# Optimization experiments

Hardware: AMD Instinct MI355X
Metric: run time of the kernel (lower is better)

Reference implementation:

```python
import jax, jax.numpy as jnp
import numpy as np

N = 50000      # nodes
E = 800000     # edges (avg degree 16)
IN = 128       # in_dim = num_heads * out_dim
H = 8          # num_heads
D = 16         # out_dim per head
R = 9          # num_rels = num_bases


def setup_inputs() -> dict:
    key = jax.random.key(0)
    ks = jax.random.split(key, 13)
    sw = 1.0 / np.sqrt(IN)
    sc = 1.0 / np.sqrt(R)
    return {
        "h": jax.random.normal(ks[0], (N, IN), jnp.float32),
        "Qw": jax.random.normal(ks[1], (R, IN, IN), jnp.float32) * sw,
        "Qc": jax.random.normal(ks[2], (R, R), jnp.float32) * sc,
        "Qb": jax.random.normal(ks[3], (IN,), jnp.float32) * 0.02,
        "Kw": jax.random.normal(ks[4], (R, IN, IN), jnp.float32) * sw,
        "Kc": jax.random.normal(ks[5], (R, R), jnp.float32) * sc,
        "Kb": jax.random.normal(ks[6], (IN,), jnp.float32) * 0.02,
        "Vw": jax.random.normal(ks[7], (R, IN, IN), jnp.float32) * sw,
        "Vc": jax.random.normal(ks[8], (R, R), jnp.float32) * sc,
        "Vb": jax.random.normal(ks[9], (IN,), jnp.float32) * 0.02,
        "src": jax.random.randint(ks[10], (E,), 0, N, jnp.int32),
        "dst": jax.random.randint(ks[11], (E,), 0, N, jnp.int32),
        "etype": jax.random.randint(ks[12], (E,), 0, R, jnp.int32),
    }


def _rel_graph_conv(x, w_basis, comb, bias, src, dst, etype):
    # basis decomposition: W_r = sum_b comb[r,b] * basis[b]  -> [R, IN, IN]
    W = jnp.einsum("rb,bio->rio", comb, w_basis)
    # project node features under every relation once: [R, N, IN]
    xW = jnp.einsum("ni,rio->rno", x, W)
    # per-edge message m_e = W_{etype_e} x_{src_e}
    msg = xW[etype, src]                                   # [E, IN]
    agg = jax.ops.segment_sum(msg, dst, num_segments=N)    # sum over incoming edges
    return jax.nn.relu(agg + bias)                         # dropout = eval mode (identity)


def reference(h, Qw, Qc, Qb, Kw, Kc, Kb, Vw, Vc, Vb, src, dst, etype):
    Q = _rel_graph_conv(h, Qw, Qc, Qb, src, dst, etype).reshape(N, H, D)
    K = _rel_graph_conv(h, Kw, Kc, Kb, src, dst, etype).reshape(N, H, D)
    V = _rel_graph_conv(h, Vw, Vc, Vb, src, dst, etype).reshape(N, H, D)
    # edge attention score: (K_src . Q_dst) per head, scaled + clamped exp
    score = jnp.sum(K[src] * Q[dst], axis=-1, keepdims=True) / np.sqrt(D)  # [E, H, 1]
    score = jnp.exp(jnp.clip(score, -10.0, 10.0))
    # weighted-V aggregation and normalizer via segment sums over dst
    wV = jax.ops.segment_sum(V[src] * score, dst, num_segments=N)  # [N, H, D]
    z = jax.ops.segment_sum(score, dst, num_segments=N)            # [N, H, 1]
    return wV / (z + 1e-6)
```

## Files before the change

### kernel.cpp

```cpp
#include <hip/hip_runtime.h>

#define NN 50000
#define NE 800000
#define IND 128
#define NH 8
#define DH 16
#define NR 9
#define KTOT 1152
#define NOUT 384
#define OB_N 24
#define NBLK 196

typedef __attribute__((ext_vector_type(8))) short bf16x8;
typedef __attribute__((ext_vector_type(4))) float f32x4;

__device__ __forceinline__ ushort f2bf(float x) {
  unsigned u = __float_as_uint(x);
  u += 0x7FFF + ((u >> 16) & 1);
  return (ushort)(u >> 16);
}
__device__ __forceinline__ float bf2f(ushort h) {
  return __uint_as_float(((unsigned)h) << 16);
}

__global__ __launch_bounds__(256) void make_w(const float* __restrict__ Qw, const float* __restrict__ Qc,
                                              const float* __restrict__ Kw, const float* __restrict__ Kc,
                                              const float* __restrict__ Vw, const float* __restrict__ Vc,
                                              ushort* __restrict__ Wh, ushort* __restrict__ Wl) {
  int t = blockIdx.x * 256 + threadIdx.x;
  int k = t / NOUT;
  int og = t % NOUT;
  int r = k >> 7, i = k & 127;
  int m = og >> 7, oc = og & 127;
  const float* basis = m == 0 ? Qw : m == 1 ? Kw : Vw;
  const float* comb  = m == 0 ? Qc : m == 1 ? Kc : Vc;
  float w = 0.f;
#pragma unroll
  for (int b = 0; b < NR; ++b)
    w += comb[r * NR + b] * basis[(long)b * IND * IND + i * IND + oc];
  ushort hi = f2bf(w);
  ushort lo = f2bf(w - bf2f(hi));
  long idx = ((long)(k >> 5) * OB_N + (og >> 4)) * 512
           + (((k >> 3) & 3) * 16 + (og & 15)) * 8 + (k & 7);
  Wh[idx] = hi;
  Wl[idx] = lo;
}

__global__ __launch_bounds__(256) void hist_dst(const int* __restrict__ dst,
                                                int* __restrict__ deg) {
  int e = blockIdx.x * 256 + threadIdx.x;
  if (e < NE) atomicAdd(&deg[dst[e]], 1);
}

__global__ __launch_bounds__(256) void scan_p1(const int* __restrict__ deg,
                                               int* __restrict__ bsum) {
  __shared__ int sb[256];
  int t = threadIdx.x;
  int idx = blockIdx.x * 256 + t;
  int v = (idx < NN) ? deg[idx] : 0;
  sb[t] = v;
  __syncthreads();
  for (int off = 128; off > 0; off >>= 1) {
    if (t < off) sb[t] += sb[t + off];
    __syncthreads();
  }
  if (t == 0) bsum[blockIdx.x] = sb[0];
}

__global__ __launch_bounds__(256) void scan_p2(const int* __restrict__ bsum,
                                               int* __restrict__ boff,
                                               int* __restrict__ rowptr) {
  __shared__ int sb[256];
  int t = threadIdx.x;
  int v = (t < NBLK) ? bsum[t] : 0;
  sb[t] = v;
  __syncthreads();
  for (int off = 1; off < 256; off <<= 1) {
    int add = (t >= off) ? sb[t - off] : 0;
    __syncthreads();
    sb[t] += add;
    __syncthreads();
  }
  if (t < NBLK) boff[t] = sb[t] - v;
  if (t == 0) rowptr[NN] = NE;
}

__global__ __launch_bounds__(256) void scan_p3(const int* __restrict__ deg,
                                               const int* __restrict__ boff,
                                               int* __restrict__ rowptr,
                                               int* __restrict__ cursor) {
  __shared__ int sb[256];
  int t = threadIdx.x;
  int idx = blockIdx.x * 256 + t;
  int v = (idx < NN) ? deg[idx] : 0;
  sb[t] = v;
  __syncthreads();
  for (int off = 1; off < 256; off <<= 1) {
    int add = (t >= off) ? sb[t - off] : 0;
    __syncthreads();
    sb[t] += add;
    __syncthreads();
  }
  if (idx < NN) {
    int excl = sb[t] - v + boff[blockIdx.x];
    rowptr[idx] = excl;
    cursor[idx] = excl;
  }
}

__global__ __launch_bounds__(256) void bucket_edges(const int* __restrict__ src,
                                                    const int* __restrict__ dst,
                                                    const int* __restrict__ et,
                                                    int* __restrict__ cursor,
                                                    int* __restrict__ epk) {
  int e = blockIdx.x * 256 + threadIdx.x;
  if (e >= NE) return;
  int d = dst[e];
  int pos = atomicAdd(&cursor[d], 1);
  epk[pos] = src[e] | (et[e] << 20);
}

__global__ __launch_bounds__(256) void conv_agg(const float* __restrict__ x,
                                                const int* __restrict__ rowptr,
                                                const int* __restrict__ epk,
                                                ushort* __restrict__ Ah,
                                                ushort* __restrict__ Al,
                                                int rlo, int rhi) {
  int wid = (blockIdx.x * 256 + threadIdx.x) >> 6;
  int lane = threadIdx.x & 63;
  if (wid >= NN) return;
  float ax[NR], ay[NR];
#pragma unroll
  for (int rr = 0; rr < NR; ++rr) { ax[rr] = 0.f; ay[rr] = 0.f; }
  int r0 = rowptr[wid], r1 = rowptr[wid + 1];
  for (int base = r0; base < r1; base += 64) {
    int pe = (base + lane < r1) ? epk[base + lane] : 0;
    int cnt = min(64, r1 - base);
    for (int j = 0; j < cnt; ++j) {
      int p = __shfl(pe, j);
      int s = p & 0xFFFFF;
      int r = p >> 20;
      float2 xv = *(const float2*)(x + (long)s * IND + lane * 2);
#pragma unroll
      for (int rr = 0; rr < NR; ++rr)
        if (r == rr) { ax[rr] += xv.x; ay[rr] += xv.y; }
    }
  }
#pragma unroll
  for (int rr = 0; rr < NR; ++rr)
    if (rr >= rlo && rr < rhi) {
      ushort h0 = f2bf(ax[rr]);
      ushort l0 = f2bf(ax[rr] - bf2f(h0));
      ushort h1 = f2bf(ay[rr]);
      ushort l1 = f2bf(ay[rr] - bf2f(h1));
      long o = ((long)(rr - rlo) * NN + wid) * IND + lane * 2;
      *(unsigned*)(Ah + o) = (unsigned)h0 | ((unsigned)h1 << 16);
      *(unsigned*)(Al + o) = (unsigned)l0 | ((unsigned)l1 << 16);
    }
}

__global__ __launch_bounds__(512) void gemm_mfma(const ushort* __restrict__ Ah,
                                                 const ushort* __restrict__ Al,
                                                 const ushort* __restrict__ Wh,
                                                 const ushort* __restrict__ Wl,
                                                 const float* __restrict__ Qb,
                                                 const float* __restrict__ Kb,
                                                 const float* __restrict__ Vb,
                                                 float* __restrict__ F,
                                                 int nrel, int rlo, int first, int last) {
  const int tid = threadIdx.x;
  const int lane = tid & 63;
  const int wid = tid >> 6;
  const int wr = wid >> 2;
  const int wc = wid & 3;
  const int n0 = blockIdx.x * 64 + wr * 32;
  const int l15 = lane & 15;
  const int kg = lane >> 4;

  const int rowA = min(n0 + l15, NN - 1);
  const int rowB = min(n0 + 16 + l15, NN - 1);

  f32x4 acc[2][6];
#pragma unroll
  for (int mi = 0; mi < 2; ++mi)
#pragma unroll
    for (int ni = 0; ni < 6; ++ni) acc[mi][ni] = (f32x4){0.f, 0.f, 0.f, 0.f};

  for (int c = 0; c < nrel; ++c) {
    const long aoff0 = ((long)c * NN + rowA) * IND + kg * 8;
    const long aoff1 = ((long)c * NN + rowB) * IND + kg * 8;
    const int kbg0 = (rlo + c) * 4;
#pragma unroll
    for (int kbl = 0; kbl < 4; ++kbl) {
      bf16x8 ah0 = *(const bf16x8*)(Ah + aoff0 + kbl * 32);
      bf16x8 ah1 = *(const bf16x8*)(Ah + aoff1 + kbl * 32);
      bf16x8 al0 = *(const bf16x8*)(Al + aoff0 + kbl * 32);
      bf16x8 al1 = *(const bf16x8*)(Al + aoff1 + kbl * 32);
#pragma unroll
      for (int ni = 0; ni < 6; ++ni) {
        const long boff = ((long)((kbg0 + kbl) * OB_N + wc * 6 + ni) * 64 + lane) * 8;
        bf16x8 bh = *(const bf16x8*)(Wh + boff);
        bf16x8 bl = *(const bf16x8*)(Wl + boff);
        acc[0][ni] = __builtin_amdgcn_mfma_f32_16x16x32_bf16(ah0, bl, acc[0][ni], 0, 0, 0);
        acc[0][ni] = __builtin_amdgcn_mfma_f32_16x16x32_bf16(al0, bh, acc[0][ni], 0, 0, 0);
        acc[0][ni] = __builtin_amdgcn_mfma_f32_16x16x32_bf16(ah0, bh, acc[0][ni], 0, 0, 0);
        acc[1][ni] = __builtin_amdgcn_mfma_f32_16x16x32_bf16(ah1, bl, acc[1][ni], 0, 0, 0);
        acc[1][ni] = __builtin_amdgcn_mfma_f32_16x16x32_bf16(al1, bh, acc[1][ni], 0, 0, 0);
        acc[1][ni] = __builtin_amdgcn_mfma_f32_16x16x32_bf16(ah1, bh, acc[1][ni], 0, 0, 0);
      }
    }
  }

#pragma unroll
  for (int mi = 0; mi < 2; ++mi) {
#pragma unroll
    for (int ni = 0; ni < 6; ++ni) {
      int og = wc * 96 + ni * 16 + l15;
      int m = og >> 7, oc = og & 127;
      float b = (m == 0 ? Qb : m == 1 ? Kb : Vb)[oc];
      float* Fm = F + (long)m * NN * IND;
#pragma unroll
      for (int reg = 0; reg < 4; ++reg) {
        int n = n0 + mi * 16 + kg * 4 + reg;
        if (n < NN) {
          long fo = (long)n * IND + oc;
          float v = acc[mi][ni][reg];
          if (!first) v += Fm[fo];
          if (last) { v += b; v = v > 0.f ? v : 0.f; }
          Fm[fo] = v;
        }
      }
    }
  }
}

__global__ __launch_bounds__(256) void node_attn(const float* __restrict__ Q,
                                                 const float* __restrict__ K,
                                                 const float* __restrict__ V,
                                                 const int* __restrict__ rowptr,
                                                 const int* __restrict__ epk,
                                                 float* __restrict__ out) {
  int wid = (blockIdx.x * 256 + threadIdx.x) >> 6;
  int lane = threadIdx.x & 63;
  if (wid >= NN) return;
  float2 q = *(const float2*)(Q + (long)wid * IND + lane * 2);
  float accx = 0.f, accy = 0.f, zacc = 0.f;
  int r0 = rowptr[wid], r1 = rowptr[wid + 1];
  for (int base = r0; base < r1; base += 64) {
    int pe = (base + lane < r1) ? epk[base + lane] : 0;
    int cnt = min(64, r1 - base);
    for (int j = 0; j < cnt; ++j) {
      int s = __shfl(pe, j) & 0xFFFFF;
      float2 k = *(const float2*)(K + (long)s * IND + lane * 2);
      float2 v = *(const float2*)(V + (long)s * IND + lane * 2);
      float p = q.x * k.x + q.y * k.y;
      p += __shfl_xor(p, 1);
      p += __shfl_xor(p, 2);
      p += __shfl_xor(p, 4);
      float score = __expf(fminf(fmaxf(p * 0.25f, -10.f), 10.f));
      accx += score * v.x;
      accy += score * v.y;
      zacc += score;
    }
  }
  float inv = 1.f / (zacc + 1e-6f);
  *(float2*)(out + (long)wid * IND + lane * 2) = make_float2(accx * inv, accy * inv);
}

extern "C" void kernel_launch(void* const* d_in, const int* in_sizes, int n_in,
                              void* d_out, int out_size, void* d_ws, size_t ws_size,
                              hipStream_t stream) {
  const float* h  = (const float*)d_in[0];
  const float* Qw = (const float*)d_in[1];
  const float* Qc = (const float*)d_in[2];
  const float* Qb = (const float*)d_in[3];
  const float* Kw = (const float*)d_in[4];
  const float* Kc = (const float*)d_in[5];
  const float* Kb = (const float*)d_in[6];
  const float* Vw = (const float*)d_in[7];
  const float* Vc = (const float*)d_in[8];
  const float* Vb = (const float*)d_in[9];
  const int* src = (const int*)d_in[10];
  const int* dst = (const int*)d_in[11];
  const int* et  = (const int*)d_in[12];
  float* out = (float*)d_out;

  char* p = (char*)d_ws;
  ushort* Wh = (ushort*)p;  p += (long)KTOT * NOUT * 2;
  ushort* Wl = (ushort*)p;  p += (long)KTOT * NOUT * 2;
  float* F   = (float*)p;   p += 3L * NN * IND * 4;
  int* deg    = (int*)p;
  int* rowptr = deg + NN;
  int* cursor = rowptr + NN + 1;
  int* bsum   = cursor + NN;
  int* boff   = bsum + NBLK;
  int* epk    = boff + NBLK;
  long intbytes = (((long)(3 * NN + 1 + 2 * NBLK + NE)) * 4 + 15) & ~15L;
  p += intbytes;
  ushort* Ah = (ushort*)p;
  long fixed = (long)(p - (char*)d_ws);
  long per_rel = 2L * NN * IND * 2;
  int C = (int)(((long)ws_size - fixed) / per_rel);
  if (C > NR) C = NR;
  if (C < 1) C = 1;
  ushort* Al = Ah + (long)C * NN * IND;

  hipMemsetAsync(deg, 0, (size_t)NN * 4, stream);

  make_w<<<(KTOT * NOUT) / 256, 256, 0, stream>>>(Qw, Qc, Kw, Kc, Vw, Vc, Wh, Wl);

  const int eb = (NE + 255) / 256;
  hist_dst<<<eb, 256, 0, stream>>>(dst, deg);
  scan_p1<<<NBLK, 256, 0, stream>>>(deg, bsum);
  scan_p2<<<1, 256, 0, stream>>>(bsum, boff, rowptr);
  scan_p3<<<NBLK, 256, 0, stream>>>(deg, boff, rowptr, cursor);
  bucket_edges<<<eb, 256, 0, stream>>>(src, dst, et, cursor, epk);

  const int nwb = (NN * 64 + 255) / 256;
  const int gb  = (NN + 63) / 64;

  int first = 1;
  for (int rlo = 0; rlo < NR; rlo += C) {
    int rhi = rlo + C;
    if (rhi > NR) rhi = NR;
    conv_agg<<<nwb, 256, 0, stream>>>(h, rowptr, epk, Ah, Al, rlo, rhi);
    gemm_mfma<<<gb, 512, 0, stream>>>(Ah, Al, Wh, Wl, Qb, Kb, Vb, F,
                                      rhi - rlo, rlo, first, (rhi == NR) ? 1 : 0);
    first = 0;
  }

  node_attn<<<nwb, 256, 0, stream>>>(F, F + (long)NN * IND, F + 2L * NN * IND,
                                     rowptr, epk, out);
}
```

Before: 915.3 us.

## Double the GEMM row tile and software-pipeline A/W register loads

The MFMA GEMM now covers 128 rows per block (64 per wave row) instead of 64, so each weight fragment loaded is reused across four row tiles rather than two. The K loop is flattened into steps and double-buffered in registers, with the next A and W fragments loaded while the current MFMAs run, to hide global-load latency. In exchange, register pressure rises considerably (96 accumulator floats plus fragment buffers), which can lower occupancy, and the grid has half as many blocks.

```diff
diff --git a/kernel.cpp b/kernel.cpp
--- a/kernel.cpp
+++ b/kernel.cpp
@@ -173,46 +173,66 @@
   const int wid = tid >> 6;
   const int wr = wid >> 2;
   const int wc = wid & 3;
-  const int n0 = blockIdx.x * 64 + wr * 32;
+  const int n0 = blockIdx.x * 128 + wr * 64;
   const int l15 = lane & 15;
   const int kg = lane >> 4;
-
-  const int rowA = min(n0 + l15, NN - 1);
-  const int rowB = min(n0 + 16 + l15, NN - 1);
-
-  f32x4 acc[2][6];
-#pragma unroll
-  for (int mi = 0; mi < 2; ++mi)
+  const int kgofs = kg * 8;
+
+  long rowOff[4];
+#pragma unroll
+  for (int mi = 0; mi < 4; ++mi)
+    rowOff[mi] = (long)min(n0 + mi * 16 + l15, NN - 1) * IND;
+
+  const int nsteps = nrel * 4;
+
+  f32x4 acc[4][6];
+#pragma unroll
+  for (int mi = 0; mi < 4; ++mi)
 #pragma unroll
     for (int ni = 0; ni < 6; ++ni) acc[mi][ni] = (f32x4){0.f, 0.f, 0.f, 0.f};
 
-  for (int c = 0; c < nrel; ++c) {
-    const long aoff0 = ((long)c * NN + rowA) * IND + kg * 8;
-    const long aoff1 = ((long)c * NN + rowB) * IND + kg * 8;
-    const int kbg0 = (rlo + c) * 4;
-#pragma unroll
-    for (int kbl = 0; kbl < 4; ++kbl) {
-      bf16x8 ah0 = *(const bf16x8*)(Ah + aoff0 + kbl * 32);
-      bf16x8 ah1 = *(const bf16x8*)(Ah + aoff1 + kbl * 32);
-      bf16x8 al0 = *(const bf16x8*)(Al + aoff0 + kbl * 32);
-      bf16x8 al1 = *(const bf16x8*)(Al + aoff1 + kbl * 32);
-#pragma unroll
-      for (int ni = 0; ni < 6; ++ni) {
-        const long boff = ((long)((kbg0 + kbl) * OB_N + wc * 6 + ni) * 64 + lane) * 8;
-        bf16x8 bh = *(const bf16x8*)(Wh + boff);
-        bf16x8 bl = *(const bf16x8*)(Wl + boff);
-        acc[0][ni] = __builtin_amdgcn_mfma_f32_16x16x32_bf16(ah0, bl, acc[0][ni], 0, 0, 0);
-        acc[0][ni] = __builtin_amdgcn_mfma_f32_16x16x32_bf16(al0, bh, acc[0][ni], 0, 0, 0);
-        acc[0][ni] = __builtin_amdgcn_mfma_f32_16x16x32_bf16(ah0, bh, acc[0][ni], 0, 0, 0);
-        acc[1][ni] = __builtin_amdgcn_mfma_f32_16x16x32_bf16(ah1, bl, acc[1][ni], 0, 0, 0);
-        acc[1][ni] = __builtin_amdgcn_mfma_f32_16x16x32_bf16(al1, bh, acc[1][ni], 0, 0, 0);
-        acc[1][ni] = __builtin_amdgcn_mfma_f32_16x16x32_bf16(ah1, bh, acc[1][ni], 0, 0, 0);
+  bf16x8 a0[8], a1[8], w[12];
+
+  auto LOADA = [&](bf16x8* A, int s) {
+    const long ab = ((long)(s >> 2) * NN) * IND + ((s & 3) * 32 + kgofs);
+#pragma unroll
+    for (int mi = 0; mi < 4; ++mi) {
+      A[mi]     = *(const bf16x8*)(Ah + ab + rowOff[mi]);
+      A[4 + mi] = *(const bf16x8*)(Al + ab + rowOff[mi]);
+    }
+  };
+  auto LOADW = [&](bf16x8* W, int s) {
+    const long wb = (((long)(rlo * 4 + s) * OB_N + wc * 6) * 64 + lane) * 8;
+#pragma unroll
+    for (int ni = 0; ni < 6; ++ni) {
+      W[ni]     = *(const bf16x8*)(Wh + wb + ni * 512);
+      W[6 + ni] = *(const bf16x8*)(Wl + wb + ni * 512);
+    }
+  };
+  auto DOMFMA = [&](bf16x8* A, bf16x8* W) {
+#pragma unroll
+    for (int ni = 0; ni < 6; ++ni)
+#pragma unroll
+      for (int mi = 0; mi < 4; ++mi) {
+        acc[mi][ni] = __builtin_amdgcn_mfma_f32_16x16x32_bf16(A[mi],     W[6 + ni], acc[mi][ni], 0, 0, 0);
+        acc[mi][ni] = __builtin_amdgcn_mfma_f32_16x16x32_bf16(A[4 + mi], W[ni],     acc[mi][ni], 0, 0, 0);
+        acc[mi][ni] = __builtin_amdgcn_mfma_f32_16x16x32_bf16(A[mi],     W[ni],     acc[mi][ni], 0, 0, 0);
       }
-    }
-  }
-
-#pragma unroll
-  for (int mi = 0; mi < 2; ++mi) {
+  };
+
+  LOADA(a0, 0);
+  LOADW(w, 0);
+  for (int s = 0; s < nsteps; s += 2) {
+    LOADA(a1, s + 1);
+    DOMFMA(a0, w);
+    LOADW(w, s + 1);
+    if (s + 2 < nsteps) LOADA(a0, s + 2);
+    DOMFMA(a1, w);
+    if (s + 2 < nsteps) LOADW(w, s + 2);
+  }
+
+#pragma unroll
+  for (int mi = 0; mi < 4; ++mi) {
 #pragma unroll
     for (int ni = 0; ni < 6; ++ni) {
       int og = wc * 96 + ni * 16 + l15;
@@ -317,7 +337,7 @@
   bucket_edges<<<eb, 256, 0, stream>>>(src, dst, et, cursor, epk);
 
   const int nwb = (NN * 64 + 255) / 256;
-  const int gb  = (NN + 63) / 64;
+  const int gb  = (NN + 127) / 128;
 
   int first = 1;
   for (int rlo = 0; rlo < NR; rlo += C) {
```

Result: faster. 764.6 us (-16.5%).
